# Performance work log

Measured on AMD Instinct MI355X. Metric: run time of the kernel, lower is better.

## Reference

```python
import jax, jax.numpy as jnp
import numpy as np
from jax import lax

EPS = 1e-5

def index_points(points, idx):
    # points [B,N,C], idx [B,...] int -> [B,...,C]
    return jax.vmap(lambda p, i: p[i])(points, idx)

def square_distance(a, b):
    # a [B,S,3], b [B,N,3] -> [B,S,N] squared euclidean
    return (jnp.sum(a * a, -1)[:, :, None] + jnp.sum(b * b, -1)[:, None, :]
            - 2.0 * jnp.einsum('bsc,bnc->bsn', a, b))

def farthest_point_sample(xyz, npoint):
    # deterministic FPS starting at index 0 (torch version starts at a random index)
    B, N, _ = xyz.shape
    def step(carry, _):
        dist, farthest = carry
        centroid = jax.vmap(lambda p, i: p[i])(xyz, farthest)  # [B,3]
        d = jnp.sum((xyz - centroid[:, None, :]) ** 2, -1)     # [B,N]
        dist = jnp.minimum(dist, d)
        nxt = jnp.argmax(dist, -1).astype(jnp.int32)
        return (dist, nxt), farthest
    init = (jnp.full((B, N), 1e10, xyz.dtype), jnp.zeros((B,), jnp.int32))
    _, idx = lax.scan(step, init, None, length=npoint)
    return jnp.transpose(idx)  # [B, npoint]

def ball_query(radius, nsample, xyz, new_xyz):
    # replicate the torch arange/mask/sort trick: first nsample in-index-order points within radius
    B, N, _ = xyz.shape
    S = new_xyz.shape[1]
    sqrdists = square_distance(new_xyz, xyz)                      # [B,S,N]
    idx = jnp.broadcast_to(jnp.arange(N, dtype=jnp.int32), (B, S, N))
    idx = jnp.where(sqrdists > radius * radius, N, idx)
    idx = jnp.sort(idx, axis=-1)[:, :, :nsample]                  # [B,S,K]
    first = idx[:, :, :1]
    return jnp.where(idx == N, first, idx)

def conv_bn_relu(x, W, b, gamma, beta):
    # 1x1 Conv2d == per-point linear; BatchNorm2d (training mode) over (B, S, K) per channel
    h = jnp.einsum('bskc,oc->bsko', x, W) + b
    mean = jnp.mean(h, axis=(0, 1, 2))
    var = jnp.var(h, axis=(0, 1, 2))
    h = (h - mean) * (gamma / jnp.sqrt(var + EPS)) + beta
    return jax.nn.relu(h)

def set_abstraction(xyz, points, npoint, radius, nsample, W, b, gamma, beta):
    fps_idx = farthest_point_sample(xyz, npoint)                  # [B,S]
    new_xyz = index_points(xyz, fps_idx)                          # [B,S,3]
    idx = ball_query(radius, nsample, xyz, new_xyz)               # [B,S,K]
    grouped_xyz = index_points(xyz, idx) - new_xyz[:, :, None, :] # [B,S,K,3]
    if points is not None:
        new_points = jnp.concatenate([grouped_xyz, index_points(points, idx)], -1)
    else:
        new_points = grouped_xyz
    h = conv_bn_relu(new_points, W, b, gamma, beta)
    return new_xyz, jnp.max(h, axis=2)                            # [B,S,Cout]

def set_abstraction_all(xyz, points, W, b, gamma, beta):
    grouped = jnp.concatenate([xyz, points], -1)[:, None]         # [B,1,N,3+C]
    h = conv_bn_relu(grouped, W, b, gamma, beta)
    return jnp.max(h, axis=2)[:, 0]                               # [B,Cout]


def setup_inputs() -> dict:
    key = jax.random.key(0)
    ks = jax.random.split(key, 6)
    B, N, Z = 8, 8192, 256
    def lin(k, o, i):
        return jax.random.normal(k, (o, i), jnp.float32) * (1.0 / np.sqrt(i))
    f32 = jnp.float32
    return {
        'xyz': jax.random.uniform(ks[0], (B, N, 3), f32),
        'w1': lin(ks[1], 128, 3),   'b1': jnp.zeros((128,), f32),
        'g1': jnp.ones((128,), f32), 'be1': jnp.zeros((128,), f32),
        'w2': lin(ks[2], 256, 131), 'b2': jnp.zeros((256,), f32),
        'g2': jnp.ones((256,), f32), 'be2': jnp.zeros((256,), f32),
        'w3': lin(ks[3], 512, 259), 'b3': jnp.zeros((512,), f32),
        'g3': jnp.ones((512,), f32), 'be3': jnp.zeros((512,), f32),
        'wf': lin(ks[4], Z, 512),   'bf': jnp.zeros((Z,), f32),
    }


def reference(xyz, w1, b1, g1, be1, w2, b2, g2, be2, w3, b3, g3, be3, wf, bf):
    # PointNet2Encoder.forward (normal_channel=False): three set-abstraction layers + fc
    l1_xyz, l1_pts = set_abstraction(xyz, None, 512, 0.2, 32, w1, b1, g1, be1)
    l2_xyz, l2_pts = set_abstraction(l1_xyz, l1_pts, 128, 0.4, 64, w2, b2, g2, be2)
    l3 = set_abstraction_all(l2_xyz, l2_pts, w3, b3, g3, be3)     # [B,512]
    return l3 @ wf.T + bf                                         # [B, z_dim]
```

## Files before the change

kernel.cpp:

```cpp
#include <hip/hip_runtime.h>
#include <hip/hip_bf16.h>
#include <cstddef>
#include <cstdint>


__device__ __forceinline__ void fma16(float* acc, float4 a, float4 b) {
  acc[0]  = fmaf(a.x, b.x, acc[0]);
  acc[1]  = fmaf(a.x, b.y, acc[1]);
  acc[2]  = fmaf(a.x, b.z, acc[2]);
  acc[3]  = fmaf(a.x, b.w, acc[3]);
  acc[4]  = fmaf(a.y, b.x, acc[4]);
  acc[5]  = fmaf(a.y, b.y, acc[5]);
  acc[6]  = fmaf(a.y, b.z, acc[6]);
  acc[7]  = fmaf(a.y, b.w, acc[7]);
  acc[8]  = fmaf(a.z, b.x, acc[8]);
  acc[9]  = fmaf(a.z, b.y, acc[9]);
  acc[10] = fmaf(a.z, b.z, acc[10]);
  acc[11] = fmaf(a.z, b.w, acc[11]);
  acc[12] = fmaf(a.w, b.x, acc[12]);
  acc[13] = fmaf(a.w, b.y, acc[13]);
  acc[14] = fmaf(a.w, b.z, acc[14]);
  acc[15] = fmaf(a.w, b.w, acc[15]);
}

#define DPP_FMAX(v, ctrl)                                                     \
  (v) = fmaxf((v), __int_as_float(__builtin_amdgcn_update_dpp(                \
                 0, __float_as_int(v), (ctrl), 0xf, 0xf, true)))

__device__ __forceinline__ float wave_max_dpp(float v) {
  DPP_FMAX(v, 0x111);
  DPP_FMAX(v, 0x112);
  DPP_FMAX(v, 0x114);
  DPP_FMAX(v, 0x118);
  DPP_FMAX(v, 0x142);
  DPP_FMAX(v, 0x143);
  return __int_as_float(__builtin_amdgcn_readlane(__float_as_int(v), 63));
}

template<int N, int NPOINT, int TPB>
__launch_bounds__(TPB)
__global__ void fps_kernel(const float* __restrict__ xyz,
                           int* __restrict__ out_idx,
                           float* __restrict__ out_xyz) {
  constexpr int PPT = N / TPB;
  constexpr int NW = TPB / 64;
  static_assert(NW == 8, "cross-wave DPP reduce assumes 8 waves");
  __shared__ float s_wval[NW];
  __shared__ float4 s_pick;
  const int b = blockIdx.x;
  const int t = threadIdx.x;
  const int lane = t & 63;
  const int wid = t >> 6;
  const float* xb = xyz + (size_t)b * N * 3;
  float px[PPT], py[PPT], pz[PPT], dist[PPT];
#pragma unroll
  for (int j = 0; j < PPT; ++j) {
    const int n = t * PPT + j;
    px[j] = xb[n * 3 + 0];
    py[j] = xb[n * 3 + 1];
    pz[j] = xb[n * 3 + 2];
    dist[j] = 1e10f;
  }
  int far = 0;
  float cx = xb[0], cy = xb[1], cz = xb[2];
  for (int i = 0; i < NPOINT; ++i) {
    if (t == 0) {
      out_idx[b * NPOINT + i] = far;
      float* o = out_xyz + ((size_t)b * NPOINT + i) * 3;
      o[0] = cx; o[1] = cy; o[2] = cz;
    }
    float m = -1.0f;
#pragma unroll
    for (int j = 0; j < PPT; ++j) {
      const float dx = __fsub_rn(px[j], cx);
      const float dy = __fsub_rn(py[j], cy);
      const float dz = __fsub_rn(pz[j], cz);
      const float d = __fadd_rn(__fadd_rn(__fmul_rn(dx, dx), __fmul_rn(dy, dy)),
                                __fmul_rn(dz, dz));
      const float nd = fminf(dist[j], d);
      dist[j] = nd;
      m = fmaxf(m, nd);
    }
    const float wv = wave_max_dpp(m);
    if (lane == 0) s_wval[wid] = wv;
    __syncthreads();
    float x = s_wval[lane & 7];
    float y = x;
    DPP_FMAX(y, 0x111);
    DPP_FMAX(y, 0x112);
    DPP_FMAX(y, 0x114);
    const float winner =
        __int_as_float(__builtin_amdgcn_readlane(__float_as_int(y), 7));
    const unsigned long long wmask = __ballot(x == winner);
    const int first_w = __ffsll(wmask) - 1;
    if (wid == first_w) {
      const unsigned long long cand = __ballot(m == winner);
      const int fl = __ffsll(cand) - 1;
      if (lane == fl) {
        int fj = 0;
        float fx = px[0], fy = py[0], fz = pz[0];
        bool found = (dist[0] == winner);
#pragma unroll
        for (int j = 1; j < PPT; ++j) {
          const bool hit = !found && (dist[j] == winner);
          if (hit) { fj = j; fx = px[j]; fy = py[j]; fz = pz[j]; found = true; }
        }
        s_pick = make_float4(__int_as_float(t * PPT + fj), fx, fy, fz);
      }
    }
    __syncthreads();
    const float4 pk = s_pick;
    far = __float_as_int(pk.x);
    cx = pk.y; cy = pk.z; cz = pk.w;
  }
}

template<int N, int S, int NS>
__global__ void ballq_kernel(const float* __restrict__ xyz,
                             const float* __restrict__ new_xyz,
                             int* __restrict__ out_idx,
                             float r2) {
  const int gw = (blockIdx.x * blockDim.x + threadIdx.x) >> 6;
  const int lane = threadIdx.x & 63;
  if (gw >= 8 * S) return;
  const int b = gw / S;
  const int s = gw % S;
  const float* c = new_xyz + ((size_t)b * S + s) * 3;
  const float cx = c[0], cy = c[1], cz = c[2];
  const float sa = __fadd_rn(__fadd_rn(__fmul_rn(cx, cx), __fmul_rn(cy, cy)),
                             __fmul_rn(cz, cz));
  const float* xb = xyz + (size_t)b * N * 3;
  int* out = out_idx + ((size_t)b * S + s) * NS;
  int cnt = 0;
  int first = -1;
  for (int n0 = 0; n0 < N && cnt < NS; n0 += 64) {
    const int n = n0 + lane;
    const float x = xb[n * 3 + 0];
    const float y = xb[n * 3 + 1];
    const float z = xb[n * 3 + 2];
    const float sb = __fadd_rn(__fadd_rn(__fmul_rn(x, x), __fmul_rn(y, y)),
                               __fmul_rn(z, z));
    const float dt = __fadd_rn(__fadd_rn(__fmul_rn(x, cx), __fmul_rn(y, cy)),
                               __fmul_rn(z, cz));
    const float d = __fsub_rn(__fadd_rn(sa, sb), __fmul_rn(2.0f, dt));
    const bool in = !(d > r2);
    const unsigned long long m = __ballot(in);
    if (in) {
      const int pos = cnt + __popcll(m & ((1ull << lane) - 1ull));
      if (pos < NS) out[pos] = n;
    }
    if (first < 0 && m) first = n0 + __ffsll((unsigned long long)m) - 1;
    cnt += __popcll(m);
  }
  for (int j = cnt + lane; j < NS; j += 64) out[j] = first;
}

__global__ void mom1_kernel(const float* __restrict__ xyz,
                            const float* __restrict__ l1_xyz,
                            const int* __restrict__ idx1,
                            float* __restrict__ part) {
  const int t = threadIdx.x;
  const int r = blockIdx.x * 256 + t;
  const int bs = r >> 5;
  const int b = r >> 14;
  const int idx = idx1[r];
  const float* p = xyz + ((size_t)(b << 13) + idx) * 3;
  const float* q = l1_xyz + (size_t)bs * 3;
  const float x = p[0] - q[0];
  const float y = p[1] - q[1];
  const float z = p[2] - q[2];
  float vals[9] = {x, y, z, x * x, x * y, x * z, y * y, y * z, z * z};
  __shared__ float sw[4][9];
  const int lane = t & 63, wid = t >> 6;
#pragma unroll
  for (int v = 0; v < 9; ++v) {
    float a = vals[v];
#pragma unroll
    for (int off = 32; off; off >>= 1) a += __shfl_xor(a, off);
    if (lane == 0) sw[wid][v] = a;
  }
  __syncthreads();
  if (t == 0) {
#pragma unroll
    for (int v = 0; v < 9; ++v)
      part[blockIdx.x * 12 + v] = sw[0][v] + sw[1][v] + sw[2][v] + sw[3][v];
  }
}

__global__ void stats1_kernel(const float* __restrict__ part,
                              const float* __restrict__ w1,
                              const float* __restrict__ b1,
                              const float* __restrict__ g1,
                              const float* __restrict__ be1,
                              float* __restrict__ ss1) {
  __shared__ double sm[9];
  const int t = threadIdx.x;
  if (t < 9) {
    double a = 0.0;
    for (int k = 0; k < 512; ++k) a += (double)part[k * 12 + t];
    sm[t] = a;
  }
  __syncthreads();
  const double n = 131072.0;
  const double mu0 = sm[0] / n, mu1 = sm[1] / n, mu2 = sm[2] / n;
  const double C00 = sm[3] / n - mu0 * mu0;
  const double C01 = sm[4] / n - mu0 * mu1;
  const double C02 = sm[5] / n - mu0 * mu2;
  const double C11 = sm[6] / n - mu1 * mu1;
  const double C12 = sm[7] / n - mu1 * mu2;
  const double C22 = sm[8] / n - mu2 * mu2;
  if (t < 128) {
    const double w0 = w1[t * 3], w1_ = w1[t * 3 + 1], w2 = w1[t * 3 + 2];
    const double mh = w0 * mu0 + w1_ * mu1 + w2 * mu2 + (double)b1[t];
    const double var = w0 * w0 * C00 + w1_ * w1_ * C11 + w2 * w2 * C22 +
                       2.0 * (w0 * w1_ * C01 + w0 * w2 * C02 + w1_ * w2 * C12);
    const float scale = g1[t] / sqrtf((float)var + 1e-5f);
    const float shift = be1[t] - (float)mh * scale;
    ss1[t * 2] = scale;
    ss1[t * 2 + 1] = shift;
  }
}

__global__ void conv1max_kernel(const float* __restrict__ xyz,
                                const float* __restrict__ l1_xyz,
                                const int* __restrict__ idx1,
                                const float* __restrict__ w1,
                                const float* __restrict__ b1,
                                const float* __restrict__ ss1,
                                float* __restrict__ l1_pts) {
  const int bs = blockIdx.x;
  const int b = bs >> 9;
  const int t = threadIdx.x;
  __shared__ float sx[32][3];
  if (t < 32) {
    const int idx = idx1[bs * 32 + t];
    const float* p = xyz + ((size_t)(b << 13) + idx) * 3;
    const float* q = l1_xyz + (size_t)bs * 3;
    sx[t][0] = p[0] - q[0];
    sx[t][1] = p[1] - q[1];
    sx[t][2] = p[2] - q[2];
  }
  __syncthreads();
  const float w0 = w1[t * 3], wa = w1[t * 3 + 1], wb = w1[t * 3 + 2];
  const float bo = b1[t];
  float hmax = -1e30f, hmin = 1e30f;
#pragma unroll 8
  for (int k = 0; k < 32; ++k) {
    const float h = sx[k][0] * w0 + sx[k][1] * wa + sx[k][2] * wb + bo;
    hmax = fmaxf(hmax, h);
    hmin = fminf(hmin, h);
  }
  const float scale = ss1[t * 2], shift = ss1[t * 2 + 1];
  const float hsel = (scale >= 0.f) ? hmax : hmin;
  l1_pts[(size_t)bs * 128 + t] = fmaxf(hsel * scale + shift, 0.0f);
}

#define MOM2_BLOCKS 256
#define MOM2_S2 (132 * 132)
#define MOM2_STRIDE (MOM2_S2 + 132)

__global__ __launch_bounds__(256)
void mom2_kernel(const float* __restrict__ l1_xyz,
                 const float* __restrict__ l1_pts,
                 const float* __restrict__ l2_xyz,
                 const int* __restrict__ idx2,
                 float* __restrict__ part) {
  __shared__ __align__(16) float xs[64 * 132];
  const int t = threadIdx.x;
  const int blk = blockIdx.x;
  float acc[5][16];
#pragma unroll
  for (int tt = 0; tt < 5; ++tt)
#pragma unroll
    for (int j = 0; j < 16; ++j) acc[tt][j] = 0.f;
  float s1 = 0.f;
  const int rbase = blk * 256;
  for (int sb = 0; sb < 4; ++sb) {
    __syncthreads();
    for (int e = t; e < 64 * 131; e += 256) {
      const int rr = e / 131, cc = e % 131;
      const int r = rbase + sb * 64 + rr;
      const int b = r >> 13;
      const int s = (r >> 6) & 127;
      const int idx = idx2[r];
      float v;
      if (cc < 3)
        v = l1_xyz[((size_t)(b << 9) + idx) * 3 + cc] -
            l2_xyz[((size_t)(b << 7) + s) * 3 + cc];
      else
        v = l1_pts[((size_t)(b << 9) + idx) * 128 + (cc - 3)];
      xs[rr * 132 + cc] = v;
    }
    if (t < 64) xs[t * 132 + 131] = 0.f;
    __syncthreads();
#pragma unroll
    for (int tt = 0; tt < 5; ++tt) {
      const int tile = t + tt * 256;
      if (tile < 33 * 33) {
        const int i0 = (tile % 33) * 4;
        const int j0 = (tile / 33) * 4;
        for (int r = 0; r < 64; ++r) {
          const float4 a = *(const float4*)&xs[r * 132 + i0];
          const float4 bb = *(const float4*)&xs[r * 132 + j0];
          fma16(acc[tt], a, bb);
        }
      }
    }
    if (t < 132) {
      for (int r = 0; r < 64; ++r) s1 += xs[r * 132 + t];
    }
  }
  float* pb = part + (size_t)blk * MOM2_STRIDE;
#pragma unroll
  for (int tt = 0; tt < 5; ++tt) {
    const int tile = t + tt * 256;
    if (tile < 33 * 33) {
      const int i0 = (tile % 33) * 4;
      const int j0 = (tile / 33) * 4;
#pragma unroll
      for (int ii = 0; ii < 4; ++ii)
#pragma unroll
        for (int jj = 0; jj < 4; ++jj)
          pb[(i0 + ii) * 132 + (j0 + jj)] = acc[tt][ii * 4 + jj];
    }
  }
  if (t < 132) pb[MOM2_S2 + t] = s1;
}

__global__ void reduce2_kernel(const float* __restrict__ part,
                               double* __restrict__ out) {
  const int e = blockIdx.x * 256 + threadIdx.x;
  if (e >= MOM2_STRIDE) return;
  double a = 0.0;
  for (int k = 0; k < MOM2_BLOCKS; ++k)
    a += (double)part[(size_t)k * MOM2_STRIDE + e];
  out[e] = a;
}

__global__ void stats2_kernel(const double* __restrict__ mom,
                              const float* __restrict__ w2,
                              const float* __restrict__ b2,
                              const float* __restrict__ g2,
                              const float* __restrict__ be2,
                              float* __restrict__ ss2) {
  const int o = blockIdx.x;
  const int t = threadIdx.x;
  const float* w = w2 + o * 131;
  double q = 0.0, md = 0.0;
  for (int i = t; i < 131; i += 128) {
    const double wi = (double)w[i];
    double di = 0.0;
    for (int j = 0; j < 131; ++j) di += mom[i * 132 + j] * (double)w[j];
    q += wi * di;
    md += wi * mom[MOM2_S2 + i];
  }
  __shared__ double sq[128], smd[128];
  sq[t] = q;
  smd[t] = md;
  __syncthreads();
  for (int off = 64; off; off >>= 1) {
    if (t < off) { sq[t] += sq[t + off]; smd[t] += smd[t + off]; }
    __syncthreads();
  }
  if (t == 0) {
    const double n = 65536.0;
    const double mdot = smd[0] / n;
    const double var = sq[0] / n - mdot * mdot;
    const double mean = mdot + (double)b2[o];
    const float scale = g2[o] / sqrtf((float)var + 1e-5f);
    const float shift = be2[o] - (float)mean * scale;
    ss2[o * 2] = scale;
    ss2[o * 2 + 1] = shift;
  }
}

__global__ __launch_bounds__(128)
void conv2max_kernel(const float* __restrict__ l1_xyz,
                     const float* __restrict__ l1_pts,
                     const float* __restrict__ l2_xyz,
                     const int* __restrict__ idx2,
                     const float* __restrict__ w2,
                     const float* __restrict__ b2,
                     const float* __restrict__ ss2,
                     float* __restrict__ l2_pts) {
  __shared__ __align__(16) float xT[131 * 68];
  __shared__ __align__(16) float wT[131 * 36];
  __shared__ float red[16 * 32];
  const int bs = blockIdx.x;
  const int b = bs >> 7;
  const int t = threadIdx.x;
  for (int e = t; e < 64 * 131; e += 128) {
    const int k = e / 131, cc = e % 131;
    const int idx = idx2[bs * 64 + k];
    float v;
    if (cc < 3)
      v = l1_xyz[((size_t)(b << 9) + idx) * 3 + cc] - l2_xyz[(size_t)bs * 3 + cc];
    else
      v = l1_pts[((size_t)(b << 9) + idx) * 128 + (cc - 3)];
    xT[cc * 68 + k] = v;
  }
  const int ty = t >> 3;
  const int tx = t & 7;
  for (int oc = 0; oc < 8; ++oc) {
    __syncthreads();
    for (int e = t; e < 32 * 131; e += 128) {
      const int oo = e / 131, cc = e % 131;
      wT[cc * 36 + oo] = w2[(oc * 32 + oo) * 131 + cc];
    }
    __syncthreads();
    float acc[16];
#pragma unroll
    for (int j = 0; j < 16; ++j) acc[j] = 0.f;
    for (int c = 0; c < 131; ++c) {
      const float4 a = *(const float4*)&xT[c * 68 + ty * 4];
      const float4 w4 = *(const float4*)&wT[c * 36 + tx * 4];
      fma16(acc, a, w4);
    }
#pragma unroll
    for (int oo = 0; oo < 4; ++oo) {
      const int o = oc * 32 + tx * 4 + oo;
      const float bo = b2[o];
      const float hmax = fmaxf(fmaxf(acc[0 + oo], acc[4 + oo]),
                               fmaxf(acc[8 + oo], acc[12 + oo])) + bo;
      const float hmin = fminf(fminf(acc[0 + oo], acc[4 + oo]),
                               fminf(acc[8 + oo], acc[12 + oo])) + bo;
      const float scale = ss2[o * 2], shift = ss2[o * 2 + 1];
      const float hsel = (scale >= 0.f) ? hmax : hmin;
      red[ty * 32 + tx * 4 + oo] = fmaxf(hsel * scale + shift, 0.f);
    }
    __syncthreads();
    if (t < 32) {
      float m = red[t];
#pragma unroll
      for (int w = 1; w < 16; ++w) m = fmaxf(m, red[w * 32 + t]);
      l2_pts[(size_t)bs * 256 + oc * 32 + t] = m;
    }
  }
}

__global__ __launch_bounds__(256)
void conv3_kernel(const float* __restrict__ l2_xyz,
                  const float* __restrict__ l2_pts,
                  const float* __restrict__ w3,
                  const float* __restrict__ b3,
                  float* __restrict__ h3T) {
  __shared__ __align__(16) float aT[96 * 68];
  __shared__ __align__(16) float wT[96 * 68];
  const int t = threadIdx.x;
  const int r0 = (blockIdx.x & 15) * 64;
  const int o0 = (blockIdx.x >> 4) * 64;
  const int ty = t >> 4, tx = t & 15;
  float acc[16];
#pragma unroll
  for (int j = 0; j < 16; ++j) acc[j] = 0.f;
  for (int c0 = 0; c0 < 259; c0 += 96) {
    __syncthreads();
    for (int e = t; e < 96 * 64; e += 256) {
      const int rr = e / 96, cc = e - rr * 96;
      const int c = c0 + cc;
      const int r = r0 + rr;
      float v = 0.f;
      if (c < 259)
        v = (c < 3) ? l2_xyz[(size_t)r * 3 + c]
                    : l2_pts[(size_t)r * 256 + (c - 3)];
      aT[cc * 68 + rr] = v;
    }
    for (int e = t; e < 96 * 64; e += 256) {
      const int oo = e / 96, cc = e - oo * 96;
      const int c = c0 + cc;
      wT[cc * 68 + oo] = (c < 259) ? w3[(size_t)(o0 + oo) * 259 + c] : 0.f;
    }
    __syncthreads();
    for (int cc = 0; cc < 96; ++cc) {
      const float4 a = *(const float4*)&aT[cc * 68 + ty * 4];
      const float4 w4 = *(const float4*)&wT[cc * 68 + tx * 4];
      fma16(acc, a, w4);
    }
  }
#pragma unroll
  for (int kk = 0; kk < 4; ++kk)
#pragma unroll
    for (int oo = 0; oo < 4; ++oo) {
      const int o = o0 + tx * 4 + oo;
      const int r = r0 + ty * 4 + kk;
      h3T[(size_t)o * 1024 + r] = acc[kk * 4 + oo] + b3[o];
    }
}

__global__ void bn3max_kernel(const float* __restrict__ h3T,
                              const float* __restrict__ g3,
                              const float* __restrict__ be3,
                              float* __restrict__ l3) {
  const int o = blockIdx.x;
  const int t = threadIdx.x;
  const float4 v = *(const float4*)&h3T[(size_t)o * 1024 + t * 4];
  double s = (double)v.x + (double)v.y + (double)v.z + (double)v.w;
  double s2 = (double)v.x * v.x + (double)v.y * v.y + (double)v.z * v.z +
              (double)v.w * v.w;
  __shared__ double sa_[256], sb_[256];
  sa_[t] = s;
  sb_[t] = s2;
  __syncthreads();
  for (int off = 128; off; off >>= 1) {
    if (t < off) { sa_[t] += sa_[t + off]; sb_[t] += sb_[t + off]; }
    __syncthreads();
  }
  const double mean = sa_[0] / 1024.0;
  const double var = sb_[0] / 1024.0 - mean * mean;
  const float scale = g3[o] / sqrtf((float)var + 1e-5f);
  const float shift = be3[o] - (float)mean * scale;
  const float hmax = fmaxf(fmaxf(v.x, v.y), fmaxf(v.z, v.w));
  const float hmin = fminf(fminf(v.x, v.y), fminf(v.z, v.w));
  const float hsel = (scale >= 0.f) ? hmax : hmin;
  __shared__ float rm[256];
  rm[t] = fmaxf(hsel * scale + shift, 0.f);
  __syncthreads();
  if (t < 8) {
    float m = rm[t * 32];
#pragma unroll
    for (int j = 1; j < 32; ++j) m = fmaxf(m, rm[t * 32 + j]);
    l3[t * 512 + o] = m;
  }
}

__global__ void final_kernel(const float* __restrict__ l3,
                             const float* __restrict__ wf,
                             const float* __restrict__ bf,
                             float* __restrict__ out) {
  const int b = blockIdx.x;
  const int t = threadIdx.x;
  __shared__ float s[512];
  s[t] = l3[b * 512 + t];
  s[t + 256] = l3[b * 512 + t + 256];
  __syncthreads();
  float acc = bf[t];
  for (int o = 0; o < 512; ++o) acc = fmaf(wf[(size_t)t * 512 + o], s[o], acc);
  out[b * 256 + t] = acc;
}

extern "C" void kernel_launch(void* const* d_in, const int* in_sizes, int n_in,
                              void* d_out, int out_size, void* d_ws, size_t ws_size,
                              hipStream_t stream) {
  (void)in_sizes; (void)n_in; (void)out_size; (void)ws_size;
  const float* xyz = (const float*)d_in[0];
  const float* w1 = (const float*)d_in[1];
  const float* b1 = (const float*)d_in[2];
  const float* g1 = (const float*)d_in[3];
  const float* be1 = (const float*)d_in[4];
  const float* w2 = (const float*)d_in[5];
  const float* b2 = (const float*)d_in[6];
  const float* g2 = (const float*)d_in[7];
  const float* be2 = (const float*)d_in[8];
  const float* w3 = (const float*)d_in[9];
  const float* b3 = (const float*)d_in[10];
  const float* g3 = (const float*)d_in[11];
  const float* be3 = (const float*)d_in[12];
  const float* wf = (const float*)d_in[13];
  const float* bf = (const float*)d_in[14];
  float* out = (float*)d_out;

  char* base = (char*)d_ws;
  size_t off = 0;
  auto alloc = [&](size_t bytes) -> char* {
    off = (off + 511) & ~(size_t)511;
    char* p = base + off;
    off += bytes;
    return p;
  };
  int* fps1_idx = (int*)alloc(8 * 512 * 4);
  float* l1_xyz = (float*)alloc(8 * 512 * 3 * 4);
  int* idx1 = (int*)alloc((size_t)8 * 512 * 32 * 4);
  float* part1 = (float*)alloc(512 * 12 * 4);
  float* ss1 = (float*)alloc(128 * 2 * 4);
  float* l1_pts = (float*)alloc((size_t)8 * 512 * 128 * 4);
  int* fps2_idx = (int*)alloc(8 * 128 * 4);
  float* l2_xyz = (float*)alloc(8 * 128 * 3 * 4);
  int* idx2 = (int*)alloc((size_t)8 * 128 * 64 * 4);
  float* part2 = (float*)alloc((size_t)MOM2_BLOCKS * MOM2_STRIDE * 4);
  double* mom2d = (double*)alloc((size_t)MOM2_STRIDE * 8);
  float* ss2 = (float*)alloc(256 * 2 * 4);
  float* l2_pts = (float*)alloc((size_t)8 * 128 * 256 * 4);
  float* h3T = (float*)alloc((size_t)512 * 1024 * 4);
  float* l3 = (float*)alloc(8 * 512 * 4);

  const float r2_1 = (float)(0.2 * 0.2);
  const float r2_2 = (float)(0.4 * 0.4);

  fps_kernel<8192, 512, 512><<<8, 512, 0, stream>>>(xyz, fps1_idx, l1_xyz);
  ballq_kernel<8192, 512, 32><<<1024, 256, 0, stream>>>(xyz, l1_xyz, idx1, r2_1);
  mom1_kernel<<<512, 256, 0, stream>>>(xyz, l1_xyz, idx1, part1);
  stats1_kernel<<<1, 128, 0, stream>>>(part1, w1, b1, g1, be1, ss1);
  conv1max_kernel<<<4096, 128, 0, stream>>>(xyz, l1_xyz, idx1, w1, b1, ss1, l1_pts);
  fps_kernel<512, 128, 512><<<8, 512, 0, stream>>>(l1_xyz, fps2_idx, l2_xyz);
  ballq_kernel<512, 128, 64><<<256, 256, 0, stream>>>(l1_xyz, l2_xyz, idx2, r2_2);
  mom2_kernel<<<MOM2_BLOCKS, 256, 0, stream>>>(l1_xyz, l1_pts, l2_xyz, idx2, part2);
  reduce2_kernel<<<(MOM2_STRIDE + 255) / 256, 256, 0, stream>>>(part2, mom2d);
  stats2_kernel<<<256, 128, 0, stream>>>(mom2d, w2, b2, g2, be2, ss2);
  conv2max_kernel<<<1024, 128, 0, stream>>>(l1_xyz, l1_pts, l2_xyz, idx2, w2, b2,
                                            ss2, l2_pts);
  conv3_kernel<<<128, 256, 0, stream>>>(l2_xyz, l2_pts, w3, b3, h3T);
  bn3max_kernel<<<512, 256, 0, stream>>>(h3T, g3, be3, l3);
  final_kernel<<<8, 256, 0, stream>>>(l3, wf, bf, out);
}
```

Before: 1.244 ms.

## Cut FPS to one barrier per iteration and pack distance math into float2

Each wave now publishes its per-wave max together with the matching point's coordinates and index into double-buffered shared memory. This removes the second __syncthreads and the serialized winner-wave candidate search from every FPS iteration. The per-point distance update is also rewritten with 2-wide float vectors so the compiler can emit packed FP32 ops, with contraction disabled to keep rounding the same. The cost is that every wave's first lane runs the candidate lookup each iteration, plus extra shared-memory stores.

```diff
diff --git a/kernel.cpp b/kernel.cpp
--- a/kernel.cpp
+++ b/kernel.cpp
@@ -3,6 +3,8 @@
 #include <cstddef>
 #include <cstdint>
 
+
+typedef float v2f __attribute__((ext_vector_type(2)));
 
 __device__ __forceinline__ void fma16(float* acc, float4 a, float4 b) {
   acc[0]  = fmaf(a.x, b.x, acc[0]);
@@ -37,6 +39,10 @@
   return __int_as_float(__builtin_amdgcn_readlane(__float_as_int(v), 63));
 }
 
+__device__ __forceinline__ float readlane_f(float v, int l) {
+  return __int_as_float(__builtin_amdgcn_readlane(__float_as_int(v), l));
+}
+
 template<int N, int NPOINT, int TPB>
 __launch_bounds__(TPB)
 __global__ void fps_kernel(const float* __restrict__ xyz,
@@ -45,22 +51,39 @@
   constexpr int PPT = N / TPB;
   constexpr int NW = TPB / 64;
   static_assert(NW == 8, "cross-wave DPP reduce assumes 8 waves");
-  __shared__ float s_wval[NW];
-  __shared__ float4 s_pick;
+  static_assert(PPT == 1 || (PPT % 2) == 0, "PPT must be 1 or even");
+  constexpr int PPT2 = (PPT >= 2) ? PPT / 2 : 1;
+  __shared__ float4 s_cand[2][NW];
+  __shared__ int s_idx[2][NW];
   const int b = blockIdx.x;
   const int t = threadIdx.x;
   const int lane = t & 63;
   const int wid = t >> 6;
   const float* xb = xyz + (size_t)b * N * 3;
-  float px[PPT], py[PPT], pz[PPT], dist[PPT];
-#pragma unroll
-  for (int j = 0; j < PPT; ++j) {
-    const int n = t * PPT + j;
-    px[j] = xb[n * 3 + 0];
-    py[j] = xb[n * 3 + 1];
-    pz[j] = xb[n * 3 + 2];
-    dist[j] = 1e10f;
-  }
+
+  v2f px2[PPT2], py2[PPT2], pz2[PPT2], dist2[PPT2];
+  float px1, py1, pz1, dist1;
+  if constexpr (PPT == 1) {
+    const int n = t;
+    px1 = xb[n * 3 + 0];
+    py1 = xb[n * 3 + 1];
+    pz1 = xb[n * 3 + 2];
+    dist1 = 1e10f;
+  } else {
+#pragma unroll
+    for (int k = 0; k < PPT2; ++k) {
+      const int n = t * PPT + 2 * k;
+      px2[k].x = xb[n * 3 + 0];
+      py2[k].x = xb[n * 3 + 1];
+      pz2[k].x = xb[n * 3 + 2];
+      px2[k].y = xb[n * 3 + 3];
+      py2[k].y = xb[n * 3 + 4];
+      pz2[k].y = xb[n * 3 + 5];
+      dist2[k].x = 1e10f;
+      dist2[k].y = 1e10f;
+    }
+  }
+
   int far = 0;
   float cx = xb[0], cy = xb[1], cz = xb[2];
   for (int i = 0; i < NPOINT; ++i) {
@@ -69,49 +92,70 @@
       float* o = out_xyz + ((size_t)b * NPOINT + i) * 3;
       o[0] = cx; o[1] = cy; o[2] = cz;
     }
-    float m = -1.0f;
-#pragma unroll
-    for (int j = 0; j < PPT; ++j) {
-      const float dx = __fsub_rn(px[j], cx);
-      const float dy = __fsub_rn(py[j], cy);
-      const float dz = __fsub_rn(pz[j], cz);
-      const float d = __fadd_rn(__fadd_rn(__fmul_rn(dx, dx), __fmul_rn(dy, dy)),
-                                __fmul_rn(dz, dz));
-      const float nd = fminf(dist[j], d);
-      dist[j] = nd;
-      m = fmaxf(m, nd);
+    float m;
+    if constexpr (PPT == 1) {
+#pragma clang fp contract(off)
+      const float dx = px1 - cx;
+      const float dy = py1 - cy;
+      const float dz = pz1 - cz;
+      const float d = dx * dx + dy * dy + dz * dz;
+      dist1 = fminf(dist1, d);
+      m = dist1;
+    } else {
+      const v2f c2x = {cx, cx}, c2y = {cy, cy}, c2z = {cz, cz};
+      v2f m2 = {-1.0f, -1.0f};
+#pragma unroll
+      for (int k = 0; k < PPT2; ++k) {
+#pragma clang fp contract(off)
+        const v2f dx = px2[k] - c2x;
+        const v2f dy = py2[k] - c2y;
+        const v2f dz = pz2[k] - c2z;
+        const v2f d = dx * dx + dy * dy + dz * dz;
+        v2f nd;
+        nd.x = fminf(dist2[k].x, d.x);
+        nd.y = fminf(dist2[k].y, d.y);
+        dist2[k] = nd;
+        m2.x = fmaxf(m2.x, nd.x);
+        m2.y = fmaxf(m2.y, nd.y);
+      }
+      m = fmaxf(m2.x, m2.y);
     }
     const float wv = wave_max_dpp(m);
-    if (lane == 0) s_wval[wid] = wv;
-    __syncthreads();
-    float x = s_wval[lane & 7];
-    float y = x;
+    const unsigned long long cand = __ballot(m == wv);
+    const int fl = __ffsll(cand) - 1;
+    const int p = i & 1;
+    if (lane == fl) {
+      int fj = 0;
+      float fx, fy, fz;
+      if constexpr (PPT == 1) {
+        fx = px1; fy = py1; fz = pz1;
+      } else {
+        fx = px2[0].x; fy = py2[0].x; fz = pz2[0].x;
+        bool found = false;
+#pragma unroll
+        for (int k = 0; k < PPT2; ++k) {
+          const bool hx = !found && (dist2[k].x == wv);
+          if (hx) { fj = 2 * k; fx = px2[k].x; fy = py2[k].x; fz = pz2[k].x; found = true; }
+          const bool hy = !found && (dist2[k].y == wv);
+          if (hy) { fj = 2 * k + 1; fx = px2[k].y; fy = py2[k].y; fz = pz2[k].y; found = true; }
+        }
+      }
+      s_cand[p][wid] = make_float4(wv, fx, fy, fz);
+      s_idx[p][wid] = t * PPT + fj;
+    }
+    __syncthreads();
+    const float4 c4 = s_cand[p][lane & 7];
+    float y = c4.x;
     DPP_FMAX(y, 0x111);
     DPP_FMAX(y, 0x112);
     DPP_FMAX(y, 0x114);
-    const float winner =
-        __int_as_float(__builtin_amdgcn_readlane(__float_as_int(y), 7));
-    const unsigned long long wmask = __ballot(x == winner);
-    const int first_w = __ffsll(wmask) - 1;
-    if (wid == first_w) {
-      const unsigned long long cand = __ballot(m == winner);
-      const int fl = __ffsll(cand) - 1;
-      if (lane == fl) {
-        int fj = 0;
-        float fx = px[0], fy = py[0], fz = pz[0];
-        bool found = (dist[0] == winner);
-#pragma unroll
-        for (int j = 1; j < PPT; ++j) {
-          const bool hit = !found && (dist[j] == winner);
-          if (hit) { fj = j; fx = px[j]; fy = py[j]; fz = pz[j]; found = true; }
-        }
-        s_pick = make_float4(__int_as_float(t * PPT + fj), fx, fy, fz);
-      }
-    }
-    __syncthreads();
-    const float4 pk = s_pick;
-    far = __float_as_int(pk.x);
-    cx = pk.y; cy = pk.z; cz = pk.w;
+    const float winner = readlane_f(y, 7);
+    const unsigned long long wmask = __ballot(c4.x == winner);
+    const int wstar = __ffsll(wmask) - 1;
+    cx = readlane_f(c4.y, wstar);
+    cy = readlane_f(c4.z, wstar);
+    cz = readlane_f(c4.w, wstar);
+    if (t == 0) far = s_idx[p][wstar];
   }
 }
 
```

Result: slower. 1.349 ms (+8.4%).

## Use single-wave FPS kernel for second set-abstraction layer

Applied to the files above, without the earlier changes.

Adds a single-wavefront farthest-point-sampling kernel in which each lane holds 8 points and the argmax is done with DPP and readlane only, with no shared memory or block barriers. It replaces the 512-thread block version for the 512-point second layer, removing two __syncthreads and the cross-wave reduction from each of the 128 serial iterations. The trade-off is less parallelism per iteration, with 8 points processed serially per lane. Ties go to the lowest lane, then the lowest j within that lane; because lanes hold contiguous index ranges, this picks the lowest index, matching the original ordering.

```diff
diff --git a/kernel.cpp b/kernel.cpp
--- a/kernel.cpp
+++ b/kernel.cpp
@@ -37,6 +37,10 @@
   return __int_as_float(__builtin_amdgcn_readlane(__float_as_int(v), 63));
 }
 
+__device__ __forceinline__ float readlane_f(float v, int l) {
+  return __int_as_float(__builtin_amdgcn_readlane(__float_as_int(v), l));
+}
+
 template<int N, int NPOINT, int TPB>
 __launch_bounds__(TPB)
 __global__ void fps_kernel(const float* __restrict__ xyz,
@@ -112,6 +116,61 @@
     const float4 pk = s_pick;
     far = __float_as_int(pk.x);
     cx = pk.y; cy = pk.z; cz = pk.w;
+  }
+}
+
+template<int N, int NPOINT>
+__launch_bounds__(64)
+__global__ void wave_fps_kernel(const float* __restrict__ xyz,
+                                int* __restrict__ out_idx,
+                                float* __restrict__ out_xyz) {
+  constexpr int PPT = N / 64;
+  const int b = blockIdx.x;
+  const int lane = threadIdx.x;
+  const float* xb = xyz + (size_t)b * N * 3;
+  float px[PPT], py[PPT], pz[PPT], dist[PPT];
+#pragma unroll
+  for (int j = 0; j < PPT; ++j) {
+    const int n = lane * PPT + j;
+    px[j] = xb[n * 3 + 0];
+    py[j] = xb[n * 3 + 1];
+    pz[j] = xb[n * 3 + 2];
+    dist[j] = 1e10f;
+  }
+  int far = 0;
+  float cx = xb[0], cy = xb[1], cz = xb[2];
+  for (int i = 0; i < NPOINT; ++i) {
+    if (lane == 0) {
+      out_idx[b * NPOINT + i] = far;
+      float* o = out_xyz + ((size_t)b * NPOINT + i) * 3;
+      o[0] = cx; o[1] = cy; o[2] = cz;
+    }
+    float m = -1.0f;
+    int mj = 0;
+    float mx = px[0], my = py[0], mz = pz[0];
+#pragma unroll
+    for (int j = 0; j < PPT; ++j) {
+      const float dx = __fsub_rn(px[j], cx);
+      const float dy = __fsub_rn(py[j], cy);
+      const float dz = __fsub_rn(pz[j], cz);
+      const float d = __fadd_rn(__fadd_rn(__fmul_rn(dx, dx), __fmul_rn(dy, dy)),
+                                __fmul_rn(dz, dz));
+      const float nd = fminf(dist[j], d);
+      dist[j] = nd;
+      const bool better = nd > m;
+      m = better ? nd : m;
+      mj = better ? j : mj;
+      mx = better ? px[j] : mx;
+      my = better ? py[j] : my;
+      mz = better ? pz[j] : mz;
+    }
+    const float wv = wave_max_dpp(m);
+    const unsigned long long cand = __ballot(m == wv);
+    const int fl = __ffsll(cand) - 1;
+    far = __builtin_amdgcn_readlane(lane * PPT + mj, fl);
+    cx = readlane_f(mx, fl);
+    cy = readlane_f(my, fl);
+    cz = readlane_f(mz, fl);
   }
 }
 
@@ -591,7 +650,7 @@
   mom1_kernel<<<512, 256, 0, stream>>>(xyz, l1_xyz, idx1, part1);
   stats1_kernel<<<1, 128, 0, stream>>>(part1, w1, b1, g1, be1, ss1);
   conv1max_kernel<<<4096, 128, 0, stream>>>(xyz, l1_xyz, idx1, w1, b1, ss1, l1_pts);
-  fps_kernel<512, 128, 512><<<8, 512, 0, stream>>>(l1_xyz, fps2_idx, l2_xyz);
+  wave_fps_kernel<512, 128><<<8, 64, 0, stream>>>(l1_xyz, fps2_idx, l2_xyz);
   ballq_kernel<512, 128, 64><<<256, 256, 0, stream>>>(l1_xyz, l2_xyz, idx2, r2_2);
   mom2_kernel<<<MOM2_BLOCKS, 256, 0, stream>>>(l1_xyz, l1_pts, l2_xyz, idx2, part2);
   reduce2_kernel<<<(MOM2_STRIDE + 255) / 256, 256, 0, stream>>>(part2, mom2d);
```

New measurement: 1.235 ms. About the same (-0.7%).
